# Kernel optimization log

Measured on AMD Instinct MI355X. Metric: run time of the kernel, lower is better.

## Reference

```python
import jax, jax.numpy as jnp
import numpy as np
import math

D_SINGLE = 384
D_PAIR = 128
N_HEADS = 12
HEAD_DIM = D_SINGLE // N_HEADS
B, L = 1, 1024
EPS = 1e-5


def _layernorm(x, g, b):
    m = jnp.mean(x, axis=-1, keepdims=True)
    v = jnp.var(x, axis=-1, keepdims=True)
    return (x - m) * jax.lax.rsqrt(v + EPS) * g + b


def setup_inputs() -> dict:
    key = jax.random.key(0)
    ks = jax.random.split(key, 12)
    std = 0.02
    return {
        "s": jax.random.normal(ks[0], (B, L, D_SINGLE), jnp.float32),
        "pair": jax.random.normal(ks[1], (B, L, L, D_PAIR), jnp.float32),
        "mask": jnp.ones((B, L), dtype=bool),
        "g_s": jnp.ones((D_SINGLE,), jnp.float32),
        "b_s": jnp.zeros((D_SINGLE,), jnp.float32),
        "Wq": jax.random.normal(ks[2], (D_SINGLE, N_HEADS * HEAD_DIM), jnp.float32) * std,
        "Wk": jax.random.normal(ks[3], (D_SINGLE, N_HEADS * HEAD_DIM), jnp.float32) * std,
        "Wv": jax.random.normal(ks[4], (D_SINGLE, N_HEADS * HEAD_DIM), jnp.float32) * std,
        "Wb": jax.random.normal(ks[5], (D_PAIR, N_HEADS), jnp.float32) * std,
        "Wo": jax.random.normal(ks[6], (N_HEADS * HEAD_DIM, D_SINGLE), jnp.float32) * std,
        "bo": jnp.zeros((D_SINGLE,), jnp.float32),
        "g_f": jnp.ones((D_SINGLE,), jnp.float32),
        "b_f": jnp.zeros((D_SINGLE,), jnp.float32),
        "W1": jax.random.normal(ks[7], (D_SINGLE, 4 * D_SINGLE), jnp.float32) * std,
        "b1": jnp.zeros((4 * D_SINGLE,), jnp.float32),
        "W2": jax.random.normal(ks[8], (4 * D_SINGLE, D_SINGLE), jnp.float32) * std,
        "b2": jnp.zeros((D_SINGLE,), jnp.float32),
    }


def reference(s, pair, mask, g_s, b_s, Wq, Wk, Wv, Wb, Wo, bo, g_f, b_f, W1, b1, W2, b2):
    Bn, Ln, _ = s.shape
    H, D = N_HEADS, HEAD_DIM
    s_norm = _layernorm(s, g_s, b_s)
    q = (s_norm @ Wq).reshape(Bn, Ln, H, D)  # [B,L,H,D]
    k = (s_norm @ Wk).reshape(Bn, Ln, H, D)
    v = (s_norm @ Wv).reshape(Bn, Ln, H, D)
    scale = 1.0 / math.sqrt(D)
    logits = jnp.einsum("bqhd,bkhd->bhqk", q, k) * scale  # [B,H,L,L]
    pair_b = jnp.einsum("bqkp,ph->bhqk", pair, Wb)
    logits = logits + pair_b
    mask2d = mask[:, None, :, None] & mask[:, None, None, :]  # [B,1,L,L]
    logits = jnp.where(mask2d, logits, -jnp.inf)
    weights = jax.nn.softmax(logits, axis=-1)
    attended = jnp.einsum("bhqk,bkhd->bqhd", weights, v).reshape(Bn, Ln, H * D)
    s = s + attended @ Wo + bo
    h = _layernorm(s, g_f, b_f)
    h = jax.nn.gelu(h @ W1 + b1, approximate=False) @ W2 + b2
    return s + h
```

## Files before the change

### kernel.cpp

```cpp
#include <hip/hip_runtime.h>
#include <hip/hip_bf16.h>
#include <math.h>

typedef short v8s __attribute__((ext_vector_type(8)));
typedef float v4f __attribute__((ext_vector_type(4)));

#define LSEQ 1024
#define DS 384
#define NH 12
#define HD 32
#define DP 128

static __device__ inline ushort f2bf(float f) {
    __hip_bfloat16 h = __float2bfloat16(f);
    return *reinterpret_cast<ushort*>(&h);
}
static __device__ inline float bf2f(ushort u) {
    return __uint_as_float(((unsigned int)u) << 16);
}
static __device__ inline float gelu_exact(float x) {
    return 0.5f * x * (1.0f + erff(x * 0.70710678118654752f));
}

__global__ __launch_bounds__(256) void prep2_k(const float* __restrict__ s,
                                               const float* __restrict__ g_s,
                                               const float* __restrict__ b_s,
                                               ushort* __restrict__ sn,
                                               const float* __restrict__ Wq,
                                               const float* __restrict__ Wk,
                                               const float* __restrict__ Wv,
                                               const float* __restrict__ Wo,
                                               const float* __restrict__ W1,
                                               const float* __restrict__ W2,
                                               ushort* __restrict__ qkvT,
                                               ushort* __restrict__ WoT,
                                               ushort* __restrict__ W1T,
                                               ushort* __restrict__ W2T,
                                               const float* __restrict__ bo,
                                               float* __restrict__ s1) {
    __shared__ float tile[32][33];
    const int bid = blockIdx.x;
    const int tid = threadIdx.x;

    if (bid < 1728) {
        int id = bid;
        const float* W; ushort* WT; int Kd, Nd, t;
        if (id < 144)       { W = Wq; WT = qkvT;             Kd = 384;  Nd = 384;  t = id; }
        else if (id < 288)  { W = Wk; WT = qkvT + 384 * 384; Kd = 384;  Nd = 384;  t = id - 144; }
        else if (id < 432)  { W = Wv; WT = qkvT + 768 * 384; Kd = 384;  Nd = 384;  t = id - 288; }
        else if (id < 576)  { W = Wo; WT = WoT;              Kd = 384;  Nd = 384;  t = id - 432; }
        else if (id < 1152) { W = W1; WT = W1T;              Kd = 384;  Nd = 1536; t = id - 576; }
        else                { W = W2; WT = W2T;              Kd = 1536; Nd = 384;  t = id - 1152; }
        const int ktiles = Kd >> 5;
        const int k0 = (t % ktiles) * 32, n0 = (t / ktiles) * 32;
        const int r = tid >> 3, c4 = (tid & 7) * 4;
        float4 v = *reinterpret_cast<const float4*>(W + (long)(k0 + r) * Nd + n0 + c4);
        tile[r][c4 + 0] = v.x; tile[r][c4 + 1] = v.y;
        tile[r][c4 + 2] = v.z; tile[r][c4 + 3] = v.w;
        __syncthreads();
        ushort4 o;
        o.x = f2bf(tile[c4 + 0][r]); o.y = f2bf(tile[c4 + 1][r]);
        o.z = f2bf(tile[c4 + 2][r]); o.w = f2bf(tile[c4 + 3][r]);
        *reinterpret_cast<ushort4*>(WT + (long)(n0 + r) * Kd + k0 + c4) = o;
    } else if (bid < 1984) {
        const int wid = tid >> 6, lane = tid & 63;
        const int row = (bid - 1728) * 4 + wid;
        const float* xr = s + (long)row * DS;
        float v[6];
        float sm = 0.f;
#pragma unroll
        for (int t = 0; t < 6; ++t) { v[t] = xr[lane + t * 64]; sm += v[t]; }
#pragma unroll
        for (int o = 32; o >= 1; o >>= 1) sm += __shfl_xor(sm, o);
        const float mean = sm * (1.f / DS);
        float q = 0.f;
#pragma unroll
        for (int t = 0; t < 6; ++t) { float d = v[t] - mean; q += d * d; }
#pragma unroll
        for (int o = 32; o >= 1; o >>= 1) q += __shfl_xor(q, o);
        const float rs = rsqrtf(q * (1.f / DS) + 1e-5f);
#pragma unroll
        for (int t = 0; t < 6; ++t) {
            int cc = lane + t * 64;
            sn[(long)row * DS + cc] = f2bf((v[t] - mean) * rs * g_s[cc] + b_s[cc]);
        }
    } else {
        const int i4 = ((bid - 1984) * 256 + tid) * 4;
        float4 sv = *reinterpret_cast<const float4*>(s + i4);
        const int col = i4 % DS;
        float4 bv = *reinterpret_cast<const float4*>(bo + col);
        float4 o;
        o.x = sv.x + bv.x; o.y = sv.y + bv.y;
        o.z = sv.z + bv.z; o.w = sv.w + bv.w;
        *reinterpret_cast<float4*>(s1 + i4) = o;
    }
}

template <int EPI>
__global__ __launch_bounds__(256) void mgemm_k(const ushort* __restrict__ A,
                                               const ushort* __restrict__ BT,
                                               float* __restrict__ Cf,
                                               ushort* __restrict__ Cb,
                                               const float* __restrict__ bias,
                                               const float* __restrict__ res,
                                               int K, int ldc, int ksplit) {
    const int w = threadIdx.x >> 6;
    const int lane = threadIdx.x & 63;
    const int c = lane & 15, g = lane >> 4;
    const int m0 = blockIdx.x * 64 + (w >> 1) * 32;
    const int n0 = blockIdx.y * 64 + (w & 1) * 32;
    const int kc = K / ksplit;
    const int kbeg = blockIdx.z * kc, kend = kbeg + kc;

    v4f acc[2][2];
#pragma unroll
    for (int i = 0; i < 2; ++i)
#pragma unroll
        for (int j = 0; j < 2; ++j) acc[i][j] = (v4f){0.f, 0.f, 0.f, 0.f};

    const ushort* Ap0 = A + (long)(m0 + c) * K + g * 8;
    const ushort* Ap1 = A + (long)(m0 + 16 + c) * K + g * 8;
    const ushort* Bp0 = BT + (long)(n0 + c) * K + g * 8;
    const ushort* Bp1 = BT + (long)(n0 + 16 + c) * K + g * 8;

#pragma unroll 4
    for (int k0 = kbeg; k0 < kend; k0 += 32) {
        v8s a0 = *reinterpret_cast<const v8s*>(Ap0 + k0);
        v8s a1 = *reinterpret_cast<const v8s*>(Ap1 + k0);
        v8s b0 = *reinterpret_cast<const v8s*>(Bp0 + k0);
        v8s b1 = *reinterpret_cast<const v8s*>(Bp1 + k0);
        acc[0][0] = __builtin_amdgcn_mfma_f32_16x16x32_bf16(a0, b0, acc[0][0], 0, 0, 0);
        acc[0][1] = __builtin_amdgcn_mfma_f32_16x16x32_bf16(a0, b1, acc[0][1], 0, 0, 0);
        acc[1][0] = __builtin_amdgcn_mfma_f32_16x16x32_bf16(a1, b0, acc[1][0], 0, 0, 0);
        acc[1][1] = __builtin_amdgcn_mfma_f32_16x16x32_bf16(a1, b1, acc[1][1], 0, 0, 0);
    }

#pragma unroll
    for (int mi = 0; mi < 2; ++mi) {
#pragma unroll
        for (int ni = 0; ni < 2; ++ni) {
#pragma unroll
            for (int r = 0; r < 4; ++r) {
                const int row = m0 + mi * 16 + g * 4 + r;
                const int col = n0 + ni * 16 + c;
                float v = acc[mi][ni][r];
                if (bias) v += bias[col];
                const long idx = (long)row * ldc + col;
                if (EPI == 1) Cf[idx] = v + res[idx];
                else if (EPI == 3) Cb[idx] = f2bf(gelu_exact(v));
                else if (EPI == 4) Cb[idx] = f2bf(v);
                else atomicAdd(&Cf[idx], v);
            }
        }
    }
}

__global__ __launch_bounds__(128) void fa2_k(const float* __restrict__ pair,
                                             const float* __restrict__ Wb,
                                             const ushort* __restrict__ qkv,
                                             ushort* __restrict__ Opart,
                                             float* __restrict__ ml) {
    __shared__ float stage[2][2][2048];
    __shared__ ushort BL[32 * 32 * 12];
    __shared__ ushort P[2][16][34];

    const int kc = blockIdx.x, qb = blockIdx.y;
    const int q0 = qb * 32, k0 = kc * 32;
    const int tid = threadIdx.x;
    const int w = tid >> 6, lane = tid & 63;
    const int c = lane & 15, g = lane >> 4;
    const float scale = 0.17677669529663688f;

    v8s bfrag[4];
#pragma unroll
    for (int t2 = 0; t2 < 4; ++t2) {
#pragma unroll
        for (int j = 0; j < 8; ++j) {
            int p = t2 * 32 + g * 8 + j;
            float wv = (c < NH) ? Wb[p * NH + c] : 0.f;
            bfrag[t2][j] = (short)f2bf(wv);
        }
    }

    const int xorkey = (c & 7) << 4;

    auto issue = [&](int t, int buf) {
        const int ql = t >> 1, kh = t & 1;
        const long tb = ((long)(q0 + w * 16 + ql) * 1024 + k0 + kh * 16) * 128;
#pragma unroll
        for (int j = 0; j < 8; ++j) {
            const int doff = j * 1024 + lane * 16;
            const int loff = doff ^ ((((doff >> 9) & 7)) << 4);
            __builtin_amdgcn_global_load_lds(
                (const __attribute__((address_space(1))) void*)((const char*)(pair + tb) + loff),
                (__attribute__((address_space(3))) void*)(&stage[w][buf][j * 256]),
                16, 0, 0);
        }
    };

    issue(0, 0);

#pragma unroll 1
    for (int t = 0; t < 32; ++t) {
        const int cur = t & 1;
        if (t < 31) {
            issue(t + 1, cur ^ 1);
            asm volatile("s_waitcnt vmcnt(8)" ::: "memory");
        } else {
            asm volatile("s_waitcnt vmcnt(0)" ::: "memory");
        }

        const int ql = t >> 1, kh = t & 1;
        const char* sw = (const char*)&stage[w][cur][0];
        v4f acc = {0.f, 0.f, 0.f, 0.f};
#pragma unroll
        for (int t2 = 0; t2 < 4; ++t2) {
            const int lo = c * 512 + t2 * 128 + g * 32;
            v4f x0 = *reinterpret_cast<const v4f*>(sw + (lo ^ xorkey));
            v4f x1 = *reinterpret_cast<const v4f*>(sw + ((lo + 16) ^ xorkey));
            v8s a;
            a[0] = (short)f2bf(x0[0]); a[1] = (short)f2bf(x0[1]);
            a[2] = (short)f2bf(x0[2]); a[3] = (short)f2bf(x0[3]);
            a[4] = (short)f2bf(x1[0]); a[5] = (short)f2bf(x1[1]);
            a[6] = (short)f2bf(x1[2]); a[7] = (short)f2bf(x1[3]);
            acc = __builtin_amdgcn_mfma_f32_16x16x32_bf16(a, bfrag[t2], acc, 0, 0, 0);
        }
        if (c < NH) {
#pragma unroll
            for (int r = 0; r < 4; ++r)
                BL[((w * 16 + ql) * 32 + kh * 16 + g * 4 + r) * 12 + c] = f2bf(acc[r]);
        }
    }

#pragma unroll 1
    for (int h = 0; h < NH; ++h) {
        const v8s aq = *reinterpret_cast<const v8s*>(
            qkv + (long)(q0 + w * 16 + c) * 1152 + h * 32 + g * 8);

        v4f sfr[2];
#pragma unroll
        for (int nf = 0; nf < 2; ++nf) {
            v8s bk = *reinterpret_cast<const v8s*>(
                qkv + (long)(k0 + nf * 16 + c) * 1152 + 384 + h * 32 + g * 8);
            v4f z = {0.f, 0.f, 0.f, 0.f};
            sfr[nf] = __builtin_amdgcn_mfma_f32_16x16x32_bf16(aq, bk, z, 0, 0, 0);
        }

        float p[2][4];
        float ls[4];
#pragma unroll
        for (int r = 0; r < 4; ++r) ls[r] = 0.f;
#pragma unroll
        for (int nf = 0; nf < 2; ++nf) {
#pragma unroll
            for (int r = 0; r < 4; ++r) {
                const int qr = w * 16 + g * 4 + r;
                float sv = sfr[nf][r] * scale + bf2f(BL[(qr * 32 + nf * 16 + c) * 12 + h]);
                float e = __expf(sv);
                p[nf][r] = e;
                ls[r] += e;
            }
        }
#pragma unroll
        for (int r = 0; r < 4; ++r) {
            ls[r] += __shfl_xor(ls[r], 1);
            ls[r] += __shfl_xor(ls[r], 2);
            ls[r] += __shfl_xor(ls[r], 4);
            ls[r] += __shfl_xor(ls[r], 8);
        }

#pragma unroll
        for (int nf = 0; nf < 2; ++nf)
#pragma unroll
            for (int r = 0; r < 4; ++r)
                P[w][g * 4 + r][nf * 16 + c] = f2bf(p[nf][r]);

        const v8s pa = *reinterpret_cast<const v8s*>(&P[w][c][g * 8]);

        v4f oacc[2];
#pragma unroll
        for (int nf2 = 0; nf2 < 2; ++nf2) {
            v8s vb;
#pragma unroll
            for (int j = 0; j < 8; ++j)
                vb[j] = (short)qkv[(long)(k0 + g * 8 + j) * 1152 + 768 + h * 32 + nf2 * 16 + c];
            v4f z = {0.f, 0.f, 0.f, 0.f};
            oacc[nf2] = __builtin_amdgcn_mfma_f32_16x16x32_bf16(pa, vb, z, 0, 0, 0);
        }

        const long base = ((long)(h * 32 + kc) * 1024 + q0 + w * 16 + g * 4);
#pragma unroll
        for (int r = 0; r < 4; ++r) {
            Opart[(base + r) * 32 + c] = f2bf(oacc[0][r]);
            Opart[(base + r) * 32 + 16 + c] = f2bf(oacc[1][r]);
        }
        if (c == 0) {
#pragma unroll
            for (int r = 0; r < 4; ++r)
                ml[base + r] = ls[r];
        }
    }
}

__global__ __launch_bounds__(256) void combine_k(const ushort* __restrict__ Opart,
                                                 const float* __restrict__ ml,
                                                 ushort* __restrict__ att) {
    const int h = blockIdx.y;
    const int q = blockIdx.x * 64 + (threadIdx.x >> 2);
    const int ds = (threadIdx.x & 3) * 8;

    float lsum = 0.f;
    float O[8];
#pragma unroll
    for (int j = 0; j < 8; ++j) O[j] = 0.f;

    for (int kc = 0; kc < 32; ++kc) {
        const long base = ((long)(h * 32 + kc) * 1024 + q);
        lsum += ml[base];
        v8s ov = *reinterpret_cast<const v8s*>(Opart + base * 32 + ds);
#pragma unroll
        for (int j = 0; j < 8; ++j) O[j] += bf2f((ushort)ov[j]);
    }
    const float inv = 1.f / lsum;
    ushort4 u0, u1;
    u0.x = f2bf(O[0] * inv); u0.y = f2bf(O[1] * inv);
    u0.z = f2bf(O[2] * inv); u0.w = f2bf(O[3] * inv);
    u1.x = f2bf(O[4] * inv); u1.y = f2bf(O[5] * inv);
    u1.z = f2bf(O[6] * inv); u1.w = f2bf(O[7] * inv);
    *reinterpret_cast<ushort4*>(att + (long)q * DS + h * 32 + ds) = u0;
    *reinterpret_cast<ushort4*>(att + (long)q * DS + h * 32 + ds + 4) = u1;
}

__global__ __launch_bounds__(256) void w1ln_k(const float* __restrict__ s1,
                                              const float* __restrict__ g_f,
                                              const float* __restrict__ b_f,
                                              const ushort* __restrict__ W1T,
                                              const float* __restrict__ b1,
                                              ushort* __restrict__ t1) {
    __shared__ ushort Abuf[64][392];
    const int tid = threadIdx.x;
    const int m0 = blockIdx.x * 64, n0 = blockIdx.y * 64;

    {
        const int row = tid >> 2, part = tid & 3;
        const float* xr = s1 + (long)(m0 + row) * DS + part * 96;
        float sum = 0.f, sq = 0.f;
#pragma unroll
        for (int i = 0; i < 24; ++i) {
            float4 v = *reinterpret_cast<const float4*>(xr + i * 4);
            sum += v.x + v.y + v.z + v.w;
            sq += v.x * v.x + v.y * v.y + v.z * v.z + v.w * v.w;
        }
        sum += __shfl_xor(sum, 1); sum += __shfl_xor(sum, 2);
        sq  += __shfl_xor(sq, 1);  sq  += __shfl_xor(sq, 2);
        const float mean = sum * (1.f / DS);
        const float var = sq * (1.f / DS) - mean * mean;
        const float rs = rsqrtf(var + 1e-5f);
#pragma unroll
        for (int i = 0; i < 24; ++i) {
            float4 v = *reinterpret_cast<const float4*>(xr + i * 4);
            const int col = part * 96 + i * 4;
            float4 gv = *reinterpret_cast<const float4*>(g_f + col);
            float4 bv = *reinterpret_cast<const float4*>(b_f + col);
            ushort4 o;
            o.x = f2bf((v.x - mean) * rs * gv.x + bv.x);
            o.y = f2bf((v.y - mean) * rs * gv.y + bv.y);
            o.z = f2bf((v.z - mean) * rs * gv.z + bv.z);
            o.w = f2bf((v.w - mean) * rs * gv.w + bv.w);
            *reinterpret_cast<ushort4*>(&Abuf[row][col]) = o;
        }
    }
    __syncthreads();

    const int w = tid >> 6;
    const int lane = tid & 63;
    const int c = lane & 15, g = lane >> 4;
    const int mloc = (w >> 1) * 32;
    const int nloc = n0 + (w & 1) * 32;

    v4f acc[2][2];
#pragma unroll
    for (int i = 0; i < 2; ++i)
#pragma unroll
        for (int j = 0; j < 2; ++j) acc[i][j] = (v4f){0.f, 0.f, 0.f, 0.f};

    const ushort* Bp0 = W1T + (long)(nloc + c) * 384 + g * 8;
    const ushort* Bp1 = W1T + (long)(nloc + 16 + c) * 384 + g * 8;

#pragma unroll 4
    for (int k0 = 0; k0 < 384; k0 += 32) {
        v8s a0 = *reinterpret_cast<const v8s*>(&Abuf[mloc + c][k0 + g * 8]);
        v8s a1 = *reinterpret_cast<const v8s*>(&Abuf[mloc + 16 + c][k0 + g * 8]);
        v8s b0 = *reinterpret_cast<const v8s*>(Bp0 + k0);
        v8s b1 = *reinterpret_cast<const v8s*>(Bp1 + k0);
        acc[0][0] = __builtin_amdgcn_mfma_f32_16x16x32_bf16(a0, b0, acc[0][0], 0, 0, 0);
        acc[0][1] = __builtin_amdgcn_mfma_f32_16x16x32_bf16(a0, b1, acc[0][1], 0, 0, 0);
        acc[1][0] = __builtin_amdgcn_mfma_f32_16x16x32_bf16(a1, b0, acc[1][0], 0, 0, 0);
        acc[1][1] = __builtin_amdgcn_mfma_f32_16x16x32_bf16(a1, b1, acc[1][1], 0, 0, 0);
    }

#pragma unroll
    for (int mi = 0; mi < 2; ++mi) {
#pragma unroll
        for (int ni = 0; ni < 2; ++ni) {
#pragma unroll
            for (int r = 0; r < 4; ++r) {
                const int row = m0 + mloc + mi * 16 + g * 4 + r;
                const int col = nloc + ni * 16 + c;
                float v = acc[mi][ni][r] + b1[col];
                t1[(long)row * 1536 + col] = f2bf(gelu_exact(v));
            }
        }
    }
}

extern "C" void kernel_launch(void* const* d_in, const int* in_sizes, int n_in,
                              void* d_out, int out_size, void* d_ws, size_t ws_size,
                              hipStream_t stream) {
    const float* s    = (const float*)d_in[0];
    const float* pair = (const float*)d_in[1];
    const float* g_s = (const float*)d_in[3];
    const float* b_s = (const float*)d_in[4];
    const float* Wq  = (const float*)d_in[5];
    const float* Wk  = (const float*)d_in[6];
    const float* Wv  = (const float*)d_in[7];
    const float* Wb  = (const float*)d_in[8];
    const float* Wo  = (const float*)d_in[9];
    const float* bo  = (const float*)d_in[10];
    const float* g_f = (const float*)d_in[11];
    const float* b_f = (const float*)d_in[12];
    const float* W1  = (const float*)d_in[13];
    const float* b1  = (const float*)d_in[14];
    const float* W2  = (const float*)d_in[15];
    const float* b2  = (const float*)d_in[16];
    float* out = (float*)d_out;

    char* ws = (char*)d_ws;
    ushort* Opart = (ushort*)ws;                       ws += 25165824;
    float*  mlb   = (float*)ws;                        ws += 1572864;
    float*  s1    = (float*)ws;                        ws += 1572864;
    ushort* qkv   = (ushort*)ws;                       ws += 2359296;
    ushort* sn    = (ushort*)ws;                       ws += 786432;
    ushort* attb  = (ushort*)ws;                       ws += 786432;
    ushort* t1    = (ushort*)ws;                       ws += 3145728;
    ushort* qkvT  = (ushort*)ws;                       ws += 884736;
    ushort* WoT   = (ushort*)ws;                       ws += 294912;
    ushort* W1T   = (ushort*)ws;                       ws += 1179648;
    ushort* W2T   = (ushort*)ws;                       ws += 1179648;

    const dim3 blk(256);

    prep2_k<<<dim3(2368), blk, 0, stream>>>(s, g_s, b_s, sn,
                                            Wq, Wk, Wv, Wo, W1, W2,
                                            qkvT, WoT, W1T, W2T, bo, s1);

    mgemm_k<4><<<dim3(16, 18, 1), blk, 0, stream>>>(sn, qkvT, nullptr, qkv,
                                                    nullptr, nullptr, 384, 1152, 1);

    fa2_k<<<dim3(32, 32), dim3(128), 0, stream>>>(pair, Wb, qkv, Opart, mlb);

    combine_k<<<dim3(16, 12), blk, 0, stream>>>(Opart, mlb, attb);

    mgemm_k<5><<<dim3(16, 6, 2), blk, 0, stream>>>(attb, WoT, s1, nullptr,
                                                   nullptr, nullptr, 384, 384, 2);

    w1ln_k<<<dim3(16, 24), blk, 0, stream>>>(s1, g_f, b_f, W1T, b1, t1);

    mgemm_k<1><<<dim3(16, 6, 1), blk, 0, stream>>>(t1, W2T, out, nullptr,
                                                   b2, s1, 1536, 384, 1);
}
```

Before: 239.1 us.

## Transpose V in QKV epilogue, single-buffer pair staging, split-K W2 with atomics

The QKV GEMM epilogue now writes V transposed into a separate buffer, so the attention kernel loads its V fragment with one vector load instead of eight strided scalar loads. The attention kernel's pair staging drops from double-buffered prefetch to a single buffer with a full wait each step, which halves LDS use but removes the overlap of loads with compute. The W2 GEMM is split four ways over K with atomic accumulation into an output that w1ln_k pre-initialises with residual plus b2, adding parallelism at the cost of atomics and nondeterministic summation order.

```diff
diff --git a/kernel.cpp b/kernel.cpp
--- a/kernel.cpp
+++ b/kernel.cpp
@@ -101,6 +101,7 @@
                                                const ushort* __restrict__ BT,
                                                float* __restrict__ Cf,
                                                ushort* __restrict__ Cb,
+                                               ushort* __restrict__ vT,
                                                const float* __restrict__ bias,
                                                const float* __restrict__ res,
                                                int K, int ldc, int ksplit) {
@@ -149,7 +150,11 @@
                 if (EPI == 1) Cf[idx] = v + res[idx];
                 else if (EPI == 3) Cb[idx] = f2bf(gelu_exact(v));
                 else if (EPI == 4) Cb[idx] = f2bf(v);
-                else atomicAdd(&Cf[idx], v);
+                else if (EPI == 5) atomicAdd(&Cf[idx], v);
+                else if (EPI == 6) {
+                    if (col < 768) Cb[idx] = f2bf(v);
+                    else vT[(long)(col - 768) * 1024 + row] = f2bf(v);
+                }
             }
         }
     }
@@ -158,9 +163,10 @@
 __global__ __launch_bounds__(128) void fa2_k(const float* __restrict__ pair,
                                              const float* __restrict__ Wb,
                                              const ushort* __restrict__ qkv,
+                                             const ushort* __restrict__ vT,
                                              ushort* __restrict__ Opart,
                                              float* __restrict__ ml) {
-    __shared__ float stage[2][2][2048];
+    __shared__ float stage[2][2048];
     __shared__ ushort BL[32 * 32 * 12];
     __shared__ ushort P[2][16][34];
 
@@ -184,34 +190,23 @@
 
     const int xorkey = (c & 7) << 4;
 
-    auto issue = [&](int t, int buf) {
+#pragma unroll 1
+    for (int t = 0; t < 32; ++t) {
         const int ql = t >> 1, kh = t & 1;
         const long tb = ((long)(q0 + w * 16 + ql) * 1024 + k0 + kh * 16) * 128;
+        asm volatile("s_waitcnt lgkmcnt(0)" ::: "memory");
 #pragma unroll
         for (int j = 0; j < 8; ++j) {
             const int doff = j * 1024 + lane * 16;
             const int loff = doff ^ ((((doff >> 9) & 7)) << 4);
             __builtin_amdgcn_global_load_lds(
                 (const __attribute__((address_space(1))) void*)((const char*)(pair + tb) + loff),
-                (__attribute__((address_space(3))) void*)(&stage[w][buf][j * 256]),
+                (__attribute__((address_space(3))) void*)(&stage[w][j * 256]),
                 16, 0, 0);
         }
-    };
-
-    issue(0, 0);
-
-#pragma unroll 1
-    for (int t = 0; t < 32; ++t) {
-        const int cur = t & 1;
-        if (t < 31) {
-            issue(t + 1, cur ^ 1);
-            asm volatile("s_waitcnt vmcnt(8)" ::: "memory");
-        } else {
-            asm volatile("s_waitcnt vmcnt(0)" ::: "memory");
-        }
-
-        const int ql = t >> 1, kh = t & 1;
-        const char* sw = (const char*)&stage[w][cur][0];
+        asm volatile("s_waitcnt vmcnt(0)" ::: "memory");
+
+        const char* sw = (const char*)&stage[w][0];
         v4f acc = {0.f, 0.f, 0.f, 0.f};
 #pragma unroll
         for (int t2 = 0; t2 < 4; ++t2) {
@@ -280,10 +275,8 @@
         v4f oacc[2];
 #pragma unroll
         for (int nf2 = 0; nf2 < 2; ++nf2) {
-            v8s vb;
-#pragma unroll
-            for (int j = 0; j < 8; ++j)
-                vb[j] = (short)qkv[(long)(k0 + g * 8 + j) * 1152 + 768 + h * 32 + nf2 * 16 + c];
+            v8s vb = *reinterpret_cast<const v8s*>(
+                vT + (long)(h * 32 + nf2 * 16 + c) * 1024 + k0 + g * 8);
             v4f z = {0.f, 0.f, 0.f, 0.f};
             oacc[nf2] = __builtin_amdgcn_mfma_f32_16x16x32_bf16(pa, vb, z, 0, 0, 0);
         }
@@ -336,6 +329,8 @@
                                               const float* __restrict__ b_f,
                                               const ushort* __restrict__ W1T,
                                               const float* __restrict__ b1,
+                                              const float* __restrict__ b2,
+                                              float* __restrict__ out,
                                               ushort* __restrict__ t1) {
     __shared__ ushort Abuf[64][392];
     const int tid = threadIdx.x;
@@ -368,6 +363,13 @@
             o.z = f2bf((v.z - mean) * rs * gv.z + bv.z);
             o.w = f2bf((v.w - mean) * rs * gv.w + bv.w);
             *reinterpret_cast<ushort4*>(&Abuf[row][col]) = o;
+            if (blockIdx.y == 0) {
+                float4 b2v = *reinterpret_cast<const float4*>(b2 + col);
+                float4 ov;
+                ov.x = v.x + b2v.x; ov.y = v.y + b2v.y;
+                ov.z = v.z + b2v.z; ov.w = v.w + b2v.w;
+                *reinterpret_cast<float4*>(out + (long)(m0 + row) * DS + col) = ov;
+            }
         }
     }
     __syncthreads();
@@ -440,6 +442,7 @@
     float*  mlb   = (float*)ws;                        ws += 1572864;
     float*  s1    = (float*)ws;                        ws += 1572864;
     ushort* qkv   = (ushort*)ws;                       ws += 2359296;
+    ushort* vTb   = (ushort*)ws;                       ws += 786432;
     ushort* sn    = (ushort*)ws;                       ws += 786432;
     ushort* attb  = (ushort*)ws;                       ws += 786432;
     ushort* t1    = (ushort*)ws;                       ws += 3145728;
@@ -454,18 +457,18 @@
                                             Wq, Wk, Wv, Wo, W1, W2,
                                             qkvT, WoT, W1T, W2T, bo, s1);
 
-    mgemm_k<4><<<dim3(16, 18, 1), blk, 0, stream>>>(sn, qkvT, nullptr, qkv,
+    mgemm_k<6><<<dim3(16, 18, 1), blk, 0, stream>>>(sn, qkvT, nullptr, qkv, vTb,
                                                     nullptr, nullptr, 384, 1152, 1);
 
-    fa2_k<<<dim3(32, 32), dim3(128), 0, stream>>>(pair, Wb, qkv, Opart, mlb);
+    fa2_k<<<dim3(32, 32), dim3(128), 0, stream>>>(pair, Wb, qkv, vTb, Opart, mlb);
 
     combine_k<<<dim3(16, 12), blk, 0, stream>>>(Opart, mlb, attb);
 
-    mgemm_k<5><<<dim3(16, 6, 2), blk, 0, stream>>>(attb, WoT, s1, nullptr,
+    mgemm_k<5><<<dim3(16, 6, 2), blk, 0, stream>>>(attb, WoT, s1, nullptr, nullptr,
                                                    nullptr, nullptr, 384, 384, 2);
 
-    w1ln_k<<<dim3(16, 24), blk, 0, stream>>>(s1, g_f, b_f, W1T, b1, t1);
-
-    mgemm_k<1><<<dim3(16, 6, 1), blk, 0, stream>>>(t1, W2T, out, nullptr,
-                                                   b2, s1, 1536, 384, 1);
-}
+    w1ln_k<<<dim3(16, 24), blk, 0, stream>>>(s1, g_f, b_f, W1T, b1, b2, out, t1);
+
+    mgemm_k<5><<<dim3(16, 6, 4), blk, 0, stream>>>(t1, W2T, out, nullptr, nullptr,
+                                                   nullptr, nullptr, 1536, 384, 4);
+}
```

After: 234.8 us. Within noise of the previous version (-1.8%).
